# Optimization experiments

Hardware: AMD Instinct MI355X
Metric: run time of the kernel (lower is better)

## Reference

```python
import jax, jax.numpy as jnp
import numpy as np

N, IN, H, D, OUT = 2048, 256, 12, 32, 384
ALPHA = 0.2


def setup_inputs() -> dict:
    key = jax.random.key(0)
    ks = jax.random.split(key, 12)
    s = 0.05
    return {
        "x": jax.random.normal(ks[0], (N, IN), jnp.float32),
        "adj": jax.random.uniform(ks[1], (N, N), jnp.float32),  # all > 0 -> fully connected mask
        "W": jax.random.normal(ks[2], (H * D, IN), jnp.float32) * s,
        "attn_src": jax.random.normal(ks[3], (H, D), jnp.float32) * s,
        "attn_dst": jax.random.normal(ks[4], (H, D), jnp.float32) * s,
        "edge_W": jax.random.normal(ks[5], (H, 1), jnp.float32) * s,
        "edge_b": jax.random.normal(ks[6], (H,), jnp.float32) * s,
        "res_W": jax.random.normal(ks[7], (H * D, IN), jnp.float32) * s,
        "res_b": jax.random.normal(ks[8], (H * D,), jnp.float32) * s,
        "fus_W": jax.random.normal(ks[9], (OUT, H * D), jnp.float32) * s,
        "fus_b": jax.random.normal(ks[10], (OUT,), jnp.float32) * s,
    }


def reference(x, adj, W, attn_src, attn_dst, edge_W, edge_b, res_W, res_b, fus_W, fus_b):
    n = x.shape[0]
    h = (x @ W.T).reshape(n, H, D)                      # [N,H,D]
    a_src = jnp.einsum("nhd,hd->nh", h, attn_src)       # [N,H]
    a_dst = jnp.einsum("nhd,hd->nh", h, attn_dst)       # [N,H]
    attn = a_src[:, None, :] + a_dst[None, :, :]        # [N,N,H]
    # edge_encoder: Linear(1 -> H) applied to adj[...,None]
    attn = attn + adj[..., None] * edge_W.reshape(1, 1, H) + edge_b
    mask = (adj > 0)[..., None]                         # [N,N,1]
    attn = jnp.where(mask, attn, -jnp.inf)
    attn = jnp.where(attn >= 0, attn, ALPHA * attn)     # leaky_relu
    attn = jax.nn.softmax(attn, axis=1)                 # over source nodes j
    # dropout is identity in eval mode
    h_out = jnp.einsum("ijh,jhd->ihd", attn, h).reshape(n, H * D)
    h_out = h_out + x @ res_W.T + res_b                 # residual
    out = jax.nn.gelu(h_out @ fus_W.T + fus_b, approximate=False)
    return out
```

## Files before the change

kernel.cpp:

```cpp
#include <hip/hip_runtime.h>
#include <hip/hip_bf16.h>

#define NN 2048
#define NH 12
#define HD 32
#define CALL 384

typedef float f32x16 __attribute__((ext_vector_type(16)));
typedef _Float16 f16x4 __attribute__((ext_vector_type(4)));
typedef __fp16 fp16x2 __attribute__((ext_vector_type(2)));

static __device__ __forceinline__ f32x16 mfma8f16(f16x4 a, f16x4 b, f32x16 c) {
    return __builtin_amdgcn_mfma_f32_32x32x8f16(a, b, c, 0, 0, 0);
}
static __device__ __forceinline__ f16x4 u2f(uint2 u) {
    union { uint2 u2; f16x4 f; } c; c.u2 = u; return c.f;
}
static __device__ __forceinline__ void gload16(const void* gp, void* lp) {
    __builtin_amdgcn_global_load_lds(
        (const __attribute__((address_space(1))) unsigned int*)gp,
        (__attribute__((address_space(3))) unsigned int*)lp, 16, 0, 0);
}

__global__ __launch_bounds__(512) void gemm01(
    const float* __restrict__ A, const float* __restrict__ B0,
    const float* __restrict__ B1, const float* __restrict__ bias1,
    const float* __restrict__ attn_src, const float* __restrict__ attn_dst,
    _Float16* __restrict__ outT, float* __restrict__ outF,
    float* __restrict__ asrc, float* __restrict__ adstT)
{
    __shared__ __align__(16) char smem[17408];
    _Float16 (*As)[68] = (_Float16(*)[68])(smem);
    _Float16 (*Bs)[68] = (_Float16(*)[68])(smem + 8704);
    float* red = (float*)smem;

    const int t = threadIdx.x;
    const int w = t >> 6, l = t & 63, g = l >> 5, il = l & 31;
    const int q = w & 3, kg = w >> 2;
    const int m0 = blockIdx.x * 64, n0 = blockIdx.y * 64;
    const int mode = blockIdx.z;
    const float* B = mode ? B1 : B0;
    const int wr = (q >> 1) * 32, wc = (q & 1) * 32;
    const int ti = t >> 3, seg = t & 7;
    const int Kdim = 256;

    const float* Abase = A + (size_t)(m0 + ti) * Kdim + seg * 8;
    const float* Bbase = B + (size_t)(n0 + ti) * Kdim + seg * 8;

    f32x16 acc;
#pragma unroll
    for (int r = 0; r < 16; ++r) acc[r] = 0.f;

    float4 av0 = *reinterpret_cast<const float4*>(Abase);
    float4 av1 = *reinterpret_cast<const float4*>(Abase + 4);
    float4 bv0 = *reinterpret_cast<const float4*>(Bbase);
    float4 bv1 = *reinterpret_cast<const float4*>(Bbase + 4);

#pragma unroll 1
    for (int ss = 0; ss < 4; ++ss) {
        __syncthreads();
        {
            f16x4 lo = {(_Float16)av0.x, (_Float16)av0.y, (_Float16)av0.z, (_Float16)av0.w};
            f16x4 hi = {(_Float16)av1.x, (_Float16)av1.y, (_Float16)av1.z, (_Float16)av1.w};
            *reinterpret_cast<f16x4*>(&As[ti][seg * 8])     = lo;
            *reinterpret_cast<f16x4*>(&As[ti][seg * 8 + 4]) = hi;
            f16x4 lo2 = {(_Float16)bv0.x, (_Float16)bv0.y, (_Float16)bv0.z, (_Float16)bv0.w};
            f16x4 hi2 = {(_Float16)bv1.x, (_Float16)bv1.y, (_Float16)bv1.z, (_Float16)bv1.w};
            *reinterpret_cast<f16x4*>(&Bs[ti][seg * 8])     = lo2;
            *reinterpret_cast<f16x4*>(&Bs[ti][seg * 8 + 4]) = hi2;
        }
        __syncthreads();
        if (ss < 3) {
            const int kk = (ss + 1) * 64;
            av0 = *reinterpret_cast<const float4*>(Abase + kk);
            av1 = *reinterpret_cast<const float4*>(Abase + kk + 4);
            bv0 = *reinterpret_cast<const float4*>(Bbase + kk);
            bv1 = *reinterpret_cast<const float4*>(Bbase + kk + 4);
        }
#pragma unroll
        for (int kc = 0; kc < 4; ++kc) {
            f16x4 af = *reinterpret_cast<const f16x4*>(&As[wr + il][kg * 32 + kc * 8 + 4 * g]);
            f16x4 bf = *reinterpret_cast<const f16x4*>(&Bs[wc + il][kg * 32 + kc * 8 + 4 * g]);
            acc = mfma8f16(af, bf, acc);
        }
    }

    __syncthreads();
    if (kg == 1) {
#pragma unroll
        for (int r = 0; r < 16; ++r) red[(q * 16 + r) * 64 + l] = acc[r];
    }
    __syncthreads();
    if (kg != 0) return;
#pragma unroll
    for (int r = 0; r < 16; ++r) acc[r] += red[(q * 16 + r) * 64 + l];

    const int colg = n0 + wc + il;
    if (mode == 0) {
#pragma unroll
        for (int p = 0; p < 4; ++p) {
            const int row = m0 + wr + 8 * p + 4 * g;
            f16x4 v;
#pragma unroll
            for (int r = 0; r < 4; ++r) v[r] = (_Float16)acc[4 * p + r];
            *reinterpret_cast<f16x4*>(&outT[(size_t)colg * NN + row]) = v;
        }
        const int hstar = colg >> 5;
        const float sv = attn_src[hstar * HD + il];
        const float dv = attn_dst[hstar * HD + il];
        float ps[16], pd[16];
#pragma unroll
        for (int r = 0; r < 16; ++r) { ps[r] = acc[r] * sv; pd[r] = acc[r] * dv; }
#pragma unroll
        for (int m = 1; m <= 16; m <<= 1) {
#pragma unroll
            for (int r = 0; r < 16; ++r) {
                ps[r] += __shfl_xor(ps[r], m);
                pd[r] += __shfl_xor(pd[r], m);
            }
        }
        if (il == 0) {
#pragma unroll
            for (int r = 0; r < 16; ++r) {
                const int row = m0 + wr + (r & 3) + 8 * (r >> 2) + 4 * g;
                asrc[row * NH + hstar] = ps[r];
                adstT[(size_t)hstar * NN + row] = pd[r] * 1.44269504089f;
            }
        }
    } else {
        const float bs = bias1[colg];
#pragma unroll
        for (int r = 0; r < 16; ++r) {
            const int row = m0 + wr + (r & 3) + 8 * (r >> 2) + 4 * g;
            outF[(size_t)row * CALL + colg] = acc[r] + bs;
        }
    }
}

__global__ __launch_bounds__(512) void gemm2(
    const _Float16* __restrict__ A16, const float* __restrict__ B,
    const float* __restrict__ bias, float* __restrict__ outF)
{
    __shared__ __align__(16) char smem[17408];
    _Float16 (*As)[68] = (_Float16(*)[68])(smem);
    _Float16 (*Bs)[68] = (_Float16(*)[68])(smem + 8704);
    float* red = (float*)smem;

    const int t = threadIdx.x;
    const int w = t >> 6, l = t & 63, g = l >> 5, il = l & 31;
    const int q = w & 3, kg = w >> 2;
    const int m0 = blockIdx.x * 64, n0 = blockIdx.y * 64;
    const int wr = (q >> 1) * 32, wc = (q & 1) * 32;
    const int ti = t >> 3, seg = t & 7;
    const int Kdim = 384;

    const _Float16* Abase = A16 + (size_t)(m0 + ti) * Kdim + seg * 8;
    const float*    Bbase = B   + (size_t)(n0 + ti) * Kdim + seg * 8;

    f32x16 acc;
#pragma unroll
    for (int r = 0; r < 16; ++r) acc[r] = 0.f;

    uint4  av = *reinterpret_cast<const uint4*>(Abase);
    float4 bv0 = *reinterpret_cast<const float4*>(Bbase);
    float4 bv1 = *reinterpret_cast<const float4*>(Bbase + 4);

#pragma unroll 1
    for (int ss = 0; ss < 6; ++ss) {
        __syncthreads();
        {
            *reinterpret_cast<uint2*>(&As[ti][seg * 8])     = make_uint2(av.x, av.y);
            *reinterpret_cast<uint2*>(&As[ti][seg * 8 + 4]) = make_uint2(av.z, av.w);
            f16x4 lo = {(_Float16)bv0.x, (_Float16)bv0.y, (_Float16)bv0.z, (_Float16)bv0.w};
            f16x4 hi = {(_Float16)bv1.x, (_Float16)bv1.y, (_Float16)bv1.z, (_Float16)bv1.w};
            *reinterpret_cast<f16x4*>(&Bs[ti][seg * 8])     = lo;
            *reinterpret_cast<f16x4*>(&Bs[ti][seg * 8 + 4]) = hi;
        }
        __syncthreads();
        if (ss < 5) {
            const int kk = (ss + 1) * 64;
            av  = *reinterpret_cast<const uint4*>(Abase + kk);
            bv0 = *reinterpret_cast<const float4*>(Bbase + kk);
            bv1 = *reinterpret_cast<const float4*>(Bbase + kk + 4);
        }
#pragma unroll
        for (int kc = 0; kc < 4; ++kc) {
            f16x4 af = *reinterpret_cast<const f16x4*>(&As[wr + il][kg * 32 + kc * 8 + 4 * g]);
            f16x4 bf = *reinterpret_cast<const f16x4*>(&Bs[wc + il][kg * 32 + kc * 8 + 4 * g]);
            acc = mfma8f16(af, bf, acc);
        }
    }

    __syncthreads();
    if (kg == 1) {
#pragma unroll
        for (int r = 0; r < 16; ++r) red[(q * 16 + r) * 64 + l] = acc[r];
    }
    __syncthreads();
    if (kg != 0) return;
#pragma unroll
    for (int r = 0; r < 16; ++r) acc[r] += red[(q * 16 + r) * 64 + l];

    const int colg = n0 + wc + il;
    const float bs = bias[colg];
#pragma unroll
    for (int r = 0; r < 16; ++r) {
        const int row = m0 + wr + (r & 3) + 8 * (r >> 2) + 4 * g;
        float vv = acc[r] + bs;
        vv = 0.5f * vv * (1.0f + erff(vv * 0.70710678118f));
        outF[(size_t)row * CALL + colg] = vv;
    }
}

__global__ __launch_bounds__(1024, 4) void attn13(
    const float* __restrict__ adj, const _Float16* __restrict__ hT,
    const float* __restrict__ asrc, const float* __restrict__ adstT,
    const float* __restrict__ eW, const float* __restrict__ eb,
    const float* __restrict__ res, _Float16* __restrict__ hsum)
{
    __shared__ __align__(16) char smem[90112];
    const int t = threadIdx.x;
    const int w = t >> 6, l = t & 63, g = l >> 5, il = l & 31;
    const int band = blockIdx.x & 63, hg = blockIdx.x >> 6;
    const int i0 = band * 32, h0 = hg * 3, c0 = hg * 96;

    char* slice   = smem + w * 5632;
    char* adjb    = slice;
    float* adst_s = (float*)(slice + 4096);
    float* red    = (float*)smem;
    float* dsum_s = (float*)(smem + 49152);

    const float LOG2E = 1.44269504089f;
    const int jbase = w * 128;
    const float* abase = adj + (size_t)(i0 + il) * NN + jbase + 16 * g;

#pragma unroll
    for (int p = 0; p < 4; ++p)
        gload16(abase + 4 * p, adjb + p * 1024);

    float base_h[3], eWr[3];
#pragma unroll
    for (int hh = 0; hh < 3; ++hh) {
        base_h[hh] = (asrc[(size_t)(i0 + il) * NH + h0 + hh] + eb[h0 + hh]) * LOG2E;
        eWr[hh] = eW[h0 + hh] * LOG2E;
    }
#pragma unroll
    for (int p = 0; p < 6; ++p) {
        const int idx = p * 64 + l;
        adst_s[idx] = adstT[(size_t)(h0 + (idx >> 7)) * NN + jbase + (idx & 127)];
    }

    f32x16 acc[3];
#pragma unroll
    for (int hh = 0; hh < 3; ++hh)
#pragma unroll
        for (int r = 0; r < 16; ++r) acc[hh][r] = 0.f;
    float4 dsumv[3];
#pragma unroll
    for (int hh = 0; hh < 3; ++hh) dsumv[hh] = make_float4(0.f, 0.f, 0.f, 0.f);

    const _Float16* hbase = hT + (size_t)(c0 + il) * NN + jbase + 16 * g;

#pragma unroll 1
    for (int tl = 0; tl < 4; ++tl) {
        const int jo = tl * 32;
        asm volatile("s_waitcnt vmcnt(0)" ::: "memory");
        const float4 aj0 = *reinterpret_cast<const float4*>(adjb + 0 * 1024 + l * 16);
        const float4 aj1 = *reinterpret_cast<const float4*>(adjb + 1 * 1024 + l * 16);
        const float4 aj2 = *reinterpret_cast<const float4*>(adjb + 2 * 1024 + l * 16);
        const float4 aj3 = *reinterpret_cast<const float4*>(adjb + 3 * 1024 + l * 16);
        asm volatile("s_waitcnt lgkmcnt(0)" ::: "memory");
        if (tl < 3) {
#pragma unroll
            for (int p = 0; p < 4; ++p)
                gload16(abase + jo + 32 + 4 * p, adjb + p * 1024);
        }
#pragma unroll
        for (int hh = 0; hh < 3; ++hh) {
            const _Float16* hp = hbase + (size_t)(hh * 32) * NN + jo;
            const uint4 hA = *reinterpret_cast<const uint4*>(hp);
            const uint4 hB = *reinterpret_cast<const uint4*>(hp + 8);
#pragma unroll
            for (int ks = 0; ks < 4; ++ks) {
                const float4 a4 = (ks == 0) ? aj0 : (ks == 1) ? aj1 : (ks == 2) ? aj2 : aj3;
                const float4 ad = *reinterpret_cast<const float4*>(
                    &adst_s[hh * 128 + jo + 16 * g + 4 * ks]);
                float e0, e1, e2, e3;
#pragma unroll
                for (int jj = 0; jj < 4; ++jj) {
                    const float ajv = (&a4.x)[jj];
                    float tt = fmaf(ajv, eWr[hh], base_h[hh] + (&ad.x)[jj]);
                    tt = fmaxf(tt, 0.2f * tt);
                    const float ee = ajv > 0.f ? __builtin_amdgcn_exp2f(tt) : 0.f;
                    (&dsumv[hh].x)[jj] += ee;
                    (jj == 0 ? e0 : jj == 1 ? e1 : jj == 2 ? e2 : e3) = ee;
                }
                union { fp16x2 h2[2]; f16x4 h4; } u;
                u.h2[0] = __builtin_amdgcn_cvt_pkrtz(e0, e1);
                u.h2[1] = __builtin_amdgcn_cvt_pkrtz(e2, e3);
                const uint2 hu = (ks == 0) ? make_uint2(hA.x, hA.y)
                               : (ks == 1) ? make_uint2(hA.z, hA.w)
                               : (ks == 2) ? make_uint2(hB.x, hB.y)
                                           : make_uint2(hB.z, hB.w);
                acc[hh] = mfma8f16(u.h4, u2f(hu), acc[hh]);
            }
        }
    }

    __syncthreads();
#pragma unroll
    for (int hh = 0; hh < 3; ++hh) {
        const float ds = (dsumv[hh].x + dsumv[hh].y) + (dsumv[hh].z + dsumv[hh].w);
        const float dtot = ds + __shfl_xor(ds, 32);
        if (g == 0) dsum_s[(w * 3 + hh) * 32 + il] = dtot;
    }
    if (w < 4) {
#pragma unroll
        for (int hh = 0; hh < 3; ++hh)
#pragma unroll
            for (int reg = 0; reg < 16; ++reg)
                red[((w * 3 + hh) * 16 + reg) * 64 + l] = acc[hh][reg];
    }
    __syncthreads();
    if (w >= 4 && w < 8) {
#pragma unroll
        for (int hh = 0; hh < 3; ++hh)
#pragma unroll
            for (int reg = 0; reg < 16; ++reg)
                red[(((w - 4) * 3 + hh) * 16 + reg) * 64 + l] += acc[hh][reg];
    }
    __syncthreads();
    if (w >= 8 && w < 12) {
#pragma unroll
        for (int hh = 0; hh < 3; ++hh)
#pragma unroll
            for (int reg = 0; reg < 16; ++reg)
                red[(((w - 8) * 3 + hh) * 16 + reg) * 64 + l] += acc[hh][reg];
    }
    __syncthreads();
    if (w >= 12) {
#pragma unroll
        for (int hh = 0; hh < 3; ++hh)
#pragma unroll
            for (int reg = 0; reg < 16; ++reg)
                red[(((w - 12) * 3 + hh) * 16 + reg) * 64 + l] += acc[hh][reg];
    }
    __syncthreads();

    {
        const int reg = w;
        const int row_off = (reg & 3) + 8 * (reg >> 2) + 4 * g;
        const int row = i0 + row_off;
#pragma unroll
        for (int hh = 0; hh < 3; ++hh) {
            float v = 0.f, d = 0.f;
#pragma unroll
            for (int p = 0; p < 4; ++p)
                v += red[((p * 3 + hh) * 16 + reg) * 64 + l];
#pragma unroll
            for (int ww = 0; ww < 16; ++ww)
                d += dsum_s[(ww * 3 + hh) * 32 + row_off];
            const int col = (h0 + hh) * 32 + il;
            hsum[(size_t)row * CALL + col] = (_Float16)(v / d + res[(size_t)row * CALL + col]);
        }
    }
}

extern "C" void kernel_launch(void* const* d_in, const int* in_sizes, int n_in,
                              void* d_out, int out_size, void* d_ws, size_t ws_size,
                              hipStream_t stream)
{
    const float* x        = (const float*)d_in[0];
    const float* adj      = (const float*)d_in[1];
    const float* W        = (const float*)d_in[2];
    const float* attn_src = (const float*)d_in[3];
    const float* attn_dst = (const float*)d_in[4];
    const float* edge_W   = (const float*)d_in[5];
    const float* edge_b   = (const float*)d_in[6];
    const float* res_W    = (const float*)d_in[7];
    const float* res_b    = (const float*)d_in[8];
    const float* fus_W    = (const float*)d_in[9];
    const float* fus_b    = (const float*)d_in[10];
    float* out = (float*)d_out;

    char* ws = (char*)d_ws;
    size_t off = 0;
    auto alloc = [&](size_t bytes) { void* p = ws + off; off = (off + bytes + 255) & ~(size_t)255; return p; };
    _Float16* hT    = (_Float16*)alloc((size_t)CALL * NN * 2);
    float*    res   = (float*)alloc((size_t)NN * CALL * 4);
    float*    asrc  = (float*)alloc((size_t)NN * NH * 4);
    float*    adstT = (float*)alloc((size_t)NH * NN * 4);
    _Float16* hsum  = (_Float16*)alloc((size_t)NN * CALL * 2);
    (void)ws_size;

    gemm01<<<dim3(32, 6, 2), dim3(512), 0, stream>>>(x, W, res_W, res_b, attn_src, attn_dst, hT, res, asrc, adstT);
    attn13<<<256, dim3(1024), 0, stream>>>(adj, hT, asrc, adstT, edge_W, edge_b, res, hsum);
    gemm2<<<dim3(32, 6), dim3(512), 0, stream>>>(hsum, fus_W, fus_b, out);
}
```

Before: 49.45 us.

## Split attention over source-node chunks with LDS double-buffering and separate combine kernel

```diff
diff --git a/kernel.cpp b/kernel.cpp
--- a/kernel.cpp
+++ b/kernel.cpp
@@ -5,6 +5,7 @@
 #define NH 12
 #define HD 32
 #define CALL 384
+#define NJS 8
 
 typedef float f32x16 __attribute__((ext_vector_type(16)));
 typedef _Float16 f16x4 __attribute__((ext_vector_type(4)));
@@ -212,158 +213,127 @@
     }
 }
 
-__global__ __launch_bounds__(1024, 4) void attn13(
+#define SLICE 38912
+__global__ __launch_bounds__(768, 6) void attn16(
     const float* __restrict__ adj, const _Float16* __restrict__ hT,
     const float* __restrict__ asrc, const float* __restrict__ adstT,
     const float* __restrict__ eW, const float* __restrict__ eb,
-    const float* __restrict__ res, _Float16* __restrict__ hsum)
-{
-    __shared__ __align__(16) char smem[90112];
+    float* __restrict__ numerP, float* __restrict__ denomP)
+{
+    __shared__ __align__(16) char smem[2 * SLICE];
     const int t = threadIdx.x;
     const int w = t >> 6, l = t & 63, g = l >> 5, il = l & 31;
-    const int band = blockIdx.x & 63, hg = blockIdx.x >> 6;
-    const int i0 = band * 32, h0 = hg * 3, c0 = hg * 96;
-
-    char* slice   = smem + w * 5632;
-    char* adjb    = slice;
-    float* adst_s = (float*)(slice + 4096);
-    float* red    = (float*)smem;
-    float* dsum_s = (float*)(smem + 49152);
+    const int band = blockIdx.x, js = blockIdx.y;
+    const int i0 = band * 32, h = w;
+    const int jbase = js * 256;
+
+    auto STAGE = [&](char* buf, int jb) {
+#pragma unroll
+        for (int e = 0; e < 2; ++e) {
+            const int p = 2 * w + e;
+            const int P = p / 6, qq = p - P * 6;
+            gload16(hT + (size_t)(qq * 64 + l) * NN + jb + P * 8,
+                    buf + 4096 + P * 8192 + qq * 1024);
+        }
+        if (w < 4)
+            gload16(adj + (size_t)(i0 + (l & 31)) * NN + jb + (2 * w + (l >> 5)) * 4,
+                    buf + w * 1024);
+        if (w == 4 || w == 5) {
+            const int e2 = w - 4;
+            const int hsrc = (e2 == 0) ? (l >> 3) : (8 + ((l >> 3) & 3));
+            gload16(adstT + (size_t)hsrc * NN + jb + (l & 7) * 4,
+                    buf + 36864 + e2 * 1024);
+        }
+    };
 
     const float LOG2E = 1.44269504089f;
-    const int jbase = w * 128;
-    const float* abase = adj + (size_t)(i0 + il) * NN + jbase + 16 * g;
-
-#pragma unroll
-    for (int p = 0; p < 4; ++p)
-        gload16(abase + 4 * p, adjb + p * 1024);
-
-    float base_h[3], eWr[3];
-#pragma unroll
-    for (int hh = 0; hh < 3; ++hh) {
-        base_h[hh] = (asrc[(size_t)(i0 + il) * NH + h0 + hh] + eb[h0 + hh]) * LOG2E;
-        eWr[hh] = eW[h0 + hh] * LOG2E;
-    }
-#pragma unroll
-    for (int p = 0; p < 6; ++p) {
-        const int idx = p * 64 + l;
-        adst_s[idx] = adstT[(size_t)(h0 + (idx >> 7)) * NN + jbase + (idx & 127)];
-    }
-
-    f32x16 acc[3];
-#pragma unroll
-    for (int hh = 0; hh < 3; ++hh)
-#pragma unroll
-        for (int r = 0; r < 16; ++r) acc[hh][r] = 0.f;
-    float4 dsumv[3];
-#pragma unroll
-    for (int hh = 0; hh < 3; ++hh) dsumv[hh] = make_float4(0.f, 0.f, 0.f, 0.f);
-
-    const _Float16* hbase = hT + (size_t)(c0 + il) * NN + jbase + 16 * g;
+    const float base = (asrc[(size_t)(i0 + il) * NH + h] + eb[h]) * LOG2E;
+    const float eWr = eW[h] * LOG2E;
+
+    f32x16 acc;
+#pragma unroll
+    for (int r = 0; r < 16; ++r) acc[r] = 0.f;
+    float4 dsum = make_float4(0.f, 0.f, 0.f, 0.f);
+
+    char* buf0 = smem;
+    char* buf1 = smem + SLICE;
+
+    STAGE(buf0, jbase);
+    asm volatile("s_waitcnt vmcnt(0)" ::: "memory");
+    __syncthreads();
 
 #pragma unroll 1
-    for (int tl = 0; tl < 4; ++tl) {
-        const int jo = tl * 32;
-        asm volatile("s_waitcnt vmcnt(0)" ::: "memory");
-        const float4 aj0 = *reinterpret_cast<const float4*>(adjb + 0 * 1024 + l * 16);
-        const float4 aj1 = *reinterpret_cast<const float4*>(adjb + 1 * 1024 + l * 16);
-        const float4 aj2 = *reinterpret_cast<const float4*>(adjb + 2 * 1024 + l * 16);
-        const float4 aj3 = *reinterpret_cast<const float4*>(adjb + 3 * 1024 + l * 16);
-        asm volatile("s_waitcnt lgkmcnt(0)" ::: "memory");
-        if (tl < 3) {
-#pragma unroll
-            for (int p = 0; p < 4; ++p)
-                gload16(abase + jo + 32 + 4 * p, adjb + p * 1024);
-        }
-#pragma unroll
-        for (int hh = 0; hh < 3; ++hh) {
-            const _Float16* hp = hbase + (size_t)(hh * 32) * NN + jo;
-            const uint4 hA = *reinterpret_cast<const uint4*>(hp);
-            const uint4 hB = *reinterpret_cast<const uint4*>(hp + 8);
-#pragma unroll
-            for (int ks = 0; ks < 4; ++ks) {
-                const float4 a4 = (ks == 0) ? aj0 : (ks == 1) ? aj1 : (ks == 2) ? aj2 : aj3;
-                const float4 ad = *reinterpret_cast<const float4*>(
-                    &adst_s[hh * 128 + jo + 16 * g + 4 * ks]);
+    for (int tl = 0; tl < 8; ++tl) {
+        char* buf  = (tl & 1) ? buf1 : buf0;
+        char* nbuf = (tl & 1) ? buf0 : buf1;
+        if (tl < 7) STAGE(nbuf, jbase + (tl + 1) * 32);
+
+        char* adjB = buf;
+        char* hTB  = buf + 4096;
+        const float* adstB = (const float*)(buf + 36864);
+#pragma unroll
+        for (int kp = 0; kp < 2; ++kp) {
+            const uint4 hv = *reinterpret_cast<const uint4*>(
+                hTB + (2 * g + kp) * 8192 + (h * 32 + il) * 16);
+#pragma unroll
+            for (int ks2 = 0; ks2 < 2; ++ks2) {
+                const int ks = 2 * kp + ks2;
+                const int G = 4 * g + ks;
+                const float4 aj = *reinterpret_cast<const float4*>(adjB + G * 512 + il * 16);
+                const float4 ad = *reinterpret_cast<const float4*>(adstB + h * 32 + G * 4);
                 float e0, e1, e2, e3;
 #pragma unroll
                 for (int jj = 0; jj < 4; ++jj) {
-                    const float ajv = (&a4.x)[jj];
-                    float tt = fmaf(ajv, eWr[hh], base_h[hh] + (&ad.x)[jj]);
+                    const float ajv = (&aj.x)[jj];
+                    float tt = fmaf(ajv, eWr, base + (&ad.x)[jj]);
                     tt = fmaxf(tt, 0.2f * tt);
                     const float ee = ajv > 0.f ? __builtin_amdgcn_exp2f(tt) : 0.f;
-                    (&dsumv[hh].x)[jj] += ee;
+                    (&dsum.x)[jj] += ee;
                     (jj == 0 ? e0 : jj == 1 ? e1 : jj == 2 ? e2 : e3) = ee;
                 }
                 union { fp16x2 h2[2]; f16x4 h4; } u;
                 u.h2[0] = __builtin_amdgcn_cvt_pkrtz(e0, e1);
                 u.h2[1] = __builtin_amdgcn_cvt_pkrtz(e2, e3);
-                const uint2 hu = (ks == 0) ? make_uint2(hA.x, hA.y)
-                               : (ks == 1) ? make_uint2(hA.z, hA.w)
-                               : (ks == 2) ? make_uint2(hB.x, hB.y)
-                                           : make_uint2(hB.z, hB.w);
-                acc[hh] = mfma8f16(u.h4, u2f(hu), acc[hh]);
+                const uint2 hu = ks2 ? make_uint2(hv.z, hv.w) : make_uint2(hv.x, hv.y);
+                acc = mfma8f16(u.h4, u2f(hu), acc);
             }
         }
-    }
-
-    __syncthreads();
-#pragma unroll
-    for (int hh = 0; hh < 3; ++hh) {
-        const float ds = (dsumv[hh].x + dsumv[hh].y) + (dsumv[hh].z + dsumv[hh].w);
-        const float dtot = ds + __shfl_xor(ds, 32);
-        if (g == 0) dsum_s[(w * 3 + hh) * 32 + il] = dtot;
-    }
-    if (w < 4) {
-#pragma unroll
-        for (int hh = 0; hh < 3; ++hh)
-#pragma unroll
-            for (int reg = 0; reg < 16; ++reg)
-                red[((w * 3 + hh) * 16 + reg) * 64 + l] = acc[hh][reg];
-    }
-    __syncthreads();
-    if (w >= 4 && w < 8) {
-#pragma unroll
-        for (int hh = 0; hh < 3; ++hh)
-#pragma unroll
-            for (int reg = 0; reg < 16; ++reg)
-                red[(((w - 4) * 3 + hh) * 16 + reg) * 64 + l] += acc[hh][reg];
-    }
-    __syncthreads();
-    if (w >= 8 && w < 12) {
-#pragma unroll
-        for (int hh = 0; hh < 3; ++hh)
-#pragma unroll
-            for (int reg = 0; reg < 16; ++reg)
-                red[(((w - 8) * 3 + hh) * 16 + reg) * 64 + l] += acc[hh][reg];
-    }
-    __syncthreads();
-    if (w >= 12) {
-#pragma unroll
-        for (int hh = 0; hh < 3; ++hh)
-#pragma unroll
-            for (int reg = 0; reg < 16; ++reg)
-                red[(((w - 12) * 3 + hh) * 16 + reg) * 64 + l] += acc[hh][reg];
-    }
-    __syncthreads();
-
-    {
-        const int reg = w;
-        const int row_off = (reg & 3) + 8 * (reg >> 2) + 4 * g;
-        const int row = i0 + row_off;
-#pragma unroll
-        for (int hh = 0; hh < 3; ++hh) {
-            float v = 0.f, d = 0.f;
-#pragma unroll
-            for (int p = 0; p < 4; ++p)
-                v += red[((p * 3 + hh) * 16 + reg) * 64 + l];
-#pragma unroll
-            for (int ww = 0; ww < 16; ++ww)
-                d += dsum_s[(ww * 3 + hh) * 32 + row_off];
-            const int col = (h0 + hh) * 32 + il;
-            hsum[(size_t)row * CALL + col] = (_Float16)(v / d + res[(size_t)row * CALL + col]);
-        }
-    }
+        asm volatile("s_waitcnt vmcnt(0)" ::: "memory");
+        __syncthreads();
+    }
+
+    float dt = (dsum.x + dsum.y) + (dsum.z + dsum.w);
+    dt += __shfl_xor(dt, 32);
+    if (l < 32)
+        denomP[(size_t)js * NN * NH + (size_t)(i0 + l) * NH + h] = dt;
+#pragma unroll
+    for (int r = 0; r < 16; ++r) {
+        const int row = (r & 3) + 8 * (r >> 2) + 4 * g;
+        numerP[(size_t)js * NN * CALL + (size_t)(i0 + row) * CALL + h * 32 + il] = acc[r];
+    }
+}
+
+__global__ __launch_bounds__(192) void combine(
+    const float* __restrict__ numerP, const float* __restrict__ denomP,
+    const float* __restrict__ res, _Float16* __restrict__ hsum)
+{
+    const int i = blockIdx.x * 2 + threadIdx.y;
+    const int c = threadIdx.x * 4;
+    const int h = c >> 5;
+    float4 s = make_float4(0.f, 0.f, 0.f, 0.f);
+    float d = 0.f;
+#pragma unroll
+    for (int js = 0; js < NJS; ++js) {
+        const float4 v = *reinterpret_cast<const float4*>(
+            numerP + (size_t)js * NN * CALL + (size_t)i * CALL + c);
+        s.x += v.x; s.y += v.y; s.z += v.z; s.w += v.w;
+        d += denomP[(size_t)js * NN * NH + (size_t)i * NH + h];
+    }
+    const float4 rv = *reinterpret_cast<const float4*>(res + (size_t)i * CALL + c);
+    const float inv = 1.0f / d;
+    f16x4 o = {(_Float16)(s.x * inv + rv.x), (_Float16)(s.y * inv + rv.y),
+               (_Float16)(s.z * inv + rv.z), (_Float16)(s.w * inv + rv.w)};
+    *reinterpret_cast<f16x4*>(hsum + (size_t)i * CALL + c) = o;
 }
 
 extern "C" void kernel_launch(void* const* d_in, const int* in_sizes, int n_in,
@@ -386,14 +356,17 @@
     char* ws = (char*)d_ws;
     size_t off = 0;
     auto alloc = [&](size_t bytes) { void* p = ws + off; off = (off + bytes + 255) & ~(size_t)255; return p; };
-    _Float16* hT    = (_Float16*)alloc((size_t)CALL * NN * 2);
-    float*    res   = (float*)alloc((size_t)NN * CALL * 4);
-    float*    asrc  = (float*)alloc((size_t)NN * NH * 4);
-    float*    adstT = (float*)alloc((size_t)NH * NN * 4);
-    _Float16* hsum  = (_Float16*)alloc((size_t)NN * CALL * 2);
+    _Float16* hT     = (_Float16*)alloc((size_t)CALL * NN * 2);
+    float*    res    = (float*)alloc((size_t)NN * CALL * 4);
+    float*    asrc   = (float*)alloc((size_t)NN * NH * 4);
+    float*    adstT  = (float*)alloc((size_t)NH * NN * 4);
+    _Float16* hsum   = (_Float16*)alloc((size_t)NN * CALL * 2);
+    float*    numerP = (float*)alloc((size_t)NJS * NN * CALL * 4);
+    float*    denomP = (float*)alloc((size_t)NJS * NN * NH * 4);
     (void)ws_size;
 
     gemm01<<<dim3(32, 6, 2), dim3(512), 0, stream>>>(x, W, res_W, res_b, attn_src, attn_dst, hT, res, asrc, adstT);
-    attn13<<<256, dim3(1024), 0, stream>>>(adj, hT, asrc, adstT, edge_W, edge_b, res, hsum);
+    attn16<<<dim3(64, NJS), dim3(768), 0, stream>>>(adj, hT, asrc, adstT, edge_W, edge_b, numerP, denomP);
+    combine<<<1024, dim3(96, 2), 0, stream>>>(numerP, denomP, res, hsum);
     gemm2<<<dim3(32, 6), dim3(512), 0, stream>>>(hsum, fus_W, fus_b, out);
 }
```

After: 61.28 us. 1.24x slower.
